# Kernel optimization log

Hardware: AMD Instinct MI355X
Metric: run time of the kernel (lower is better)

The kernel has to match this reference:

```python
import jax, jax.numpy as jnp
import numpy as np

B, NPG, C = 256, 256, 256  # graphs, nodes-per-graph, in_channels
MAX_LEN = 500


def _sinusoid_pe(max_len, c):
    pos = np.arange(max_len, dtype=np.float32)[:, None]
    div = np.exp(np.arange(0, c, 2, dtype=np.float32) * (-np.log(10000.0) / c))
    pe = np.zeros((max_len, c), np.float32)
    pe[:, 0::2] = np.sin(pos * div)
    pe[:, 1::2] = np.cos(pos * div)
    return jnp.asarray(pe)


def setup_inputs() -> dict:
    key = jax.random.key(0)
    ks = jax.random.split(key, 8)
    N = B * NPG
    x = jax.random.normal(ks[0], (N, C), jnp.float32)
    batch = jnp.repeat(jnp.arange(B, dtype=jnp.int32), NPG)
    # every other atom in each graph is an N/O atom -> 128 per graph
    on_index = (jnp.arange(B, dtype=jnp.int32)[:, None] * NPG
                + jnp.arange(0, NPG, 2, dtype=jnp.int32)[None, :]).reshape(-1)
    W1 = jax.random.normal(ks[1], (C, 256), jnp.float32) / np.sqrt(C)
    b1 = jnp.zeros((256,), jnp.float32)
    W2 = jax.random.normal(ks[2], (256, 128), jnp.float32) / np.sqrt(256.0)
    b2 = jnp.zeros((128,), jnp.float32)
    W3 = jax.random.normal(ks[3], (128, 64), jnp.float32) / np.sqrt(128.0)
    b3 = jnp.zeros((64,), jnp.float32)
    w_atom = jax.random.normal(ks[4], (64,), jnp.float32) / 8.0
    return {"x": x, "pe": _sinusoid_pe(MAX_LEN, C), "W1": W1, "b1": b1,
            "W2": W2, "b2": b2, "W3": W3, "b3": b3, "w_atom": w_atom,
            "batch": batch, "on_index": on_index, "ratio": 16}


def _lrelu(z):
    return jnp.where(z > 0, z, 0.1 * z)


def reference(x, pe, W1, b1, W2, b2, W3, b3, w_atom, batch, on_index, ratio):
    N = x.shape[0]
    bsz = int(batch[-1]) + 1
    num_nodes = jax.ops.segment_sum(jnp.ones_like(batch), batch, num_segments=bsz)
    cum = jnp.concatenate([jnp.zeros((1,), batch.dtype), jnp.cumsum(num_nodes)[:-1]])
    n = int(num_nodes.max())  # max_num_nodes
    idx_in_graph = jnp.arange(N, dtype=batch.dtype) - cum[batch]
    # positional encoding (dropout = identity in eval)
    xp = x + pe[idx_in_graph]
    # scoring MLP
    h = _lrelu(xp @ W1 + b1)
    h = _lrelu(h @ W2 + b2)
    h = _lrelu(h @ W3 + b3)
    score = jnp.tanh((h * w_atom).sum(-1) / jnp.linalg.norm(w_atom))
    # dense-pack scores into [bsz, n] padded with -inf, sort descending per row
    dense_idx = jnp.arange(N, dtype=batch.dtype) - cum[batch] + batch * n
    dense = jnp.full((bsz * n,), jnp.finfo(x.dtype).min, x.dtype).at[dense_idx].set(score)
    order = jnp.argsort(-dense.reshape(bsz, n), axis=-1)       # perm within row
    ranks = jnp.argsort(order, axis=-1)                         # inverse perm
    pos_in_perm = (jnp.arange(bsz)[:, None] * n + ranks).reshape(-1)
    # positions (in the flattened perm) of N/O atoms, sorted -> grouped per graph
    on_par = dense_idx[on_index]                                # padded/parallel ids
    indices = jnp.sort(pos_in_perm[on_par])
    m = on_index.shape[0] // bsz                                # N/O atoms per graph (uniform here)
    k = min(int(ratio), m)                                      # k = min(ratio, on_num)
    pre_mask = (jnp.arange(bsz)[:, None] * m + jnp.arange(k)[None, :]).reshape(-1)
    mask = indices[pre_mask]
    # map padded indices back to global node ids (subtract cumulative void counts)
    void = n - num_nodes
    cum_void = jnp.concatenate([jnp.zeros((1,), batch.dtype), jnp.cumsum(void)[:-1]])
    perm_flat = (order + (jnp.arange(bsz) * n - cum_void)[:, None]).reshape(-1)
    perm = perm_flat[mask]
    x_top = (xp[perm] * score[perm][:, None]).reshape(bsz, int(ratio), -1)
    return (x_top, perm, score[on_index], on_index)
```

## Files before the change

### kernel.cpp

```cpp
#include <hip/hip_runtime.h>
#include <hip/hip_bf16.h>


typedef __attribute__((ext_vector_type(8))) short short8v;
typedef __attribute__((ext_vector_type(4))) float float4v;

#define W1P_OFF 0
#define W2P_OFF 131072
#define W3P_OFF 196608
#define SCORES_OFF 212992

static __device__ __forceinline__ float lrelu(float z) { return z > 0.0f ? z : 0.1f * z; }

static __device__ __forceinline__ short f2bf(float f) {
    union { float f; unsigned u; } v; v.f = f;
    const unsigned r = v.u + 0x7FFFu + ((v.u >> 16) & 1u);
    return (short)(r >> 16);
}

static __device__ __forceinline__ int sw_off(int row, int chunk, int within) {
    return row * 256 + ((chunk ^ (row & 7)) << 3) + within;
}

__global__ __launch_bounds__(256) void pack_kernel(
    const float* __restrict__ W1, const float* __restrict__ W2,
    const float* __restrict__ W3, short* __restrict__ ws)
{
    const int u = blockIdx.x * 256 + threadIdx.x;
    if (u >= 13312) return;
    const float* W; int N, unitBase, uu;
    short* dst;
    if (u < 8192)       { W = W1; N = 256; uu = u;         dst = ws + (W1P_OFF/2); unitBase = 8; }
    else if (u < 12288) { W = W2; N = 128; uu = u - 8192;  dst = ws + (W2P_OFF/2); unitBase = 8; }
    else                { W = W3; N = 64;  uu = u - 12288; dst = ws + (W3P_OFF/2); unitBase = 4; }
    const int perNt = unitBase * 64;
    const int nt   = uu / perNt;
    const int rem  = uu % perNt;
    const int ks   = rem / 64;
    const int lane = rem % 64;
    const int q = lane >> 4;
    const int n = nt * 16 + (lane & 15);
    short8v frag;
    #pragma unroll
    for (int j = 0; j < 8; ++j) {
        const int k = ks * 32 + q * 8 + j;
        frag[j] = f2bf(W[(size_t)k * N + n]);
    }
    *(short8v*)(dst + (size_t)uu * 8) = frag;
}

__global__ __launch_bounds__(256, 5) void mlp_score_kernel(
    const float* __restrict__ x, const float* __restrict__ pe,
    const float* __restrict__ b1, const float* __restrict__ b2,
    const float* __restrict__ b3, const float* __restrict__ w_atom,
    const int* __restrict__ on_index, const short* __restrict__ ws_pack,
    float* __restrict__ ws_scores,
    float* __restrict__ out_score, float* __restrict__ out_onidx)
{
    __shared__ __align__(16) short XP[32 * 256];
    __shared__ __align__(16) short H1[32 * 256];
    const int t   = threadIdx.x;
    const int m0  = blockIdx.x * 32;
    const int wid = t >> 6;
    const int lane = t & 63;
    const int q = lane >> 4;
    const int c = lane & 15;

    const short* W1p = ws_pack + (W1P_OFF / 2);
    const short* W2p = ws_pack + (W2P_OFF / 2);
    const short* W3p = ws_pack + (W3P_OFF / 2);

    #pragma unroll
    for (int i = 0; i < 4; ++i) {
        const int u = t + i * 256;
        const int r = u >> 5;
        const int ck = u & 31;
        const int k = ck << 3;
        const int node = on_index[m0 + r];
        const float4 xa = *(const float4*)(x + (size_t)node * 256 + k);
        const float4 xb = *(const float4*)(x + (size_t)node * 256 + k + 4);
        const float4 pa = *(const float4*)(pe + (size_t)(node & 255) * 256 + k);
        const float4 pb = *(const float4*)(pe + (size_t)(node & 255) * 256 + k + 4);
        short8v s;
        s[0] = f2bf(xa.x + pa.x); s[1] = f2bf(xa.y + pa.y);
        s[2] = f2bf(xa.z + pa.z); s[3] = f2bf(xa.w + pa.w);
        s[4] = f2bf(xb.x + pb.x); s[5] = f2bf(xb.y + pb.y);
        s[6] = f2bf(xb.z + pb.z); s[7] = f2bf(xb.w + pb.w);
        *(short8v*)(&XP[sw_off(r, ck, 0)]) = s;
    }
    __syncthreads();

    #pragma unroll
    for (int g = 0; g < 2; ++g) {
        const int ntA = wid * 4 + g * 2;
        float4v acc[2][2];
        #pragma unroll
        for (int nt = 0; nt < 2; ++nt) {
            const float bb = b1[(ntA + nt) * 16 + c];
            acc[0][nt] = (float4v){bb, bb, bb, bb};
            acc[1][nt] = (float4v){bb, bb, bb, bb};
        }
        #pragma unroll
        for (int ks = 0; ks < 8; ++ks) {
            const short8v a0 = *(const short8v*)(&XP[sw_off(c,      ks * 4 + q, 0)]);
            const short8v a1 = *(const short8v*)(&XP[sw_off(16 + c, ks * 4 + q, 0)]);
            #pragma unroll
            for (int nt = 0; nt < 2; ++nt) {
                const short8v b = *(const short8v*)(W1p + ((size_t)((ntA + nt) * 8 + ks) * 64 + lane) * 8);
                acc[0][nt] = __builtin_amdgcn_mfma_f32_16x16x32_bf16(a0, b, acc[0][nt], 0, 0, 0);
                acc[1][nt] = __builtin_amdgcn_mfma_f32_16x16x32_bf16(a1, b, acc[1][nt], 0, 0, 0);
            }
        }
        #pragma unroll
        for (int mt = 0; mt < 2; ++mt)
            #pragma unroll
            for (int nt = 0; nt < 2; ++nt)
                #pragma unroll
                for (int r = 0; r < 4; ++r) {
                    const int row = mt * 16 + q * 4 + r;
                    const int col = (ntA + nt) * 16 + c;
                    H1[sw_off(row, col >> 3, col & 7)] = f2bf(lrelu(acc[mt][nt][r]));
                }
    }
    __syncthreads();

    {
        const int nt0 = wid * 2;
        float4v acc[2][2];
        #pragma unroll
        for (int nt = 0; nt < 2; ++nt) {
            const float bb = b2[(nt0 + nt) * 16 + c];
            acc[0][nt] = (float4v){bb, bb, bb, bb};
            acc[1][nt] = (float4v){bb, bb, bb, bb};
        }
        #pragma unroll
        for (int ks = 0; ks < 8; ++ks) {
            const short8v a0 = *(const short8v*)(&H1[sw_off(c,      ks * 4 + q, 0)]);
            const short8v a1 = *(const short8v*)(&H1[sw_off(16 + c, ks * 4 + q, 0)]);
            #pragma unroll
            for (int nt = 0; nt < 2; ++nt) {
                const short8v b = *(const short8v*)(W2p + ((size_t)((nt0 + nt) * 8 + ks) * 64 + lane) * 8);
                acc[0][nt] = __builtin_amdgcn_mfma_f32_16x16x32_bf16(a0, b, acc[0][nt], 0, 0, 0);
                acc[1][nt] = __builtin_amdgcn_mfma_f32_16x16x32_bf16(a1, b, acc[1][nt], 0, 0, 0);
            }
        }
        __syncthreads();
        #pragma unroll
        for (int mt = 0; mt < 2; ++mt)
            #pragma unroll
            for (int nt = 0; nt < 2; ++nt)
                #pragma unroll
                for (int r = 0; r < 4; ++r) {
                    const int row = mt * 16 + q * 4 + r;
                    const int col = (nt0 + nt) * 16 + c;
                    XP[sw_off(row, col >> 3, col & 7)] = f2bf(lrelu(acc[mt][nt][r]));
                }
    }
    __syncthreads();

    {
        const int nt = wid;
        float4v acc[2];
        const float bb = b3[nt * 16 + c];
        acc[0] = (float4v){bb, bb, bb, bb};
        acc[1] = (float4v){bb, bb, bb, bb};
        #pragma unroll
        for (int ks = 0; ks < 4; ++ks) {
            const short8v a0 = *(const short8v*)(&XP[sw_off(c,      ks * 4 + q, 0)]);
            const short8v a1 = *(const short8v*)(&XP[sw_off(16 + c, ks * 4 + q, 0)]);
            const short8v b = *(const short8v*)(W3p + ((size_t)(nt * 4 + ks) * 64 + lane) * 8);
            acc[0] = __builtin_amdgcn_mfma_f32_16x16x32_bf16(a0, b, acc[0], 0, 0, 0);
            acc[1] = __builtin_amdgcn_mfma_f32_16x16x32_bf16(a1, b, acc[1], 0, 0, 0);
        }
        float* H3F = (float*)H1;
        #pragma unroll
        for (int mt = 0; mt < 2; ++mt)
            #pragma unroll
            for (int r = 0; r < 4; ++r)
                H3F[(mt * 16 + q * 4 + r) * 68 + nt * 16 + c] = lrelu(acc[mt][r]);
    }
    __syncthreads();

    {
        const float* H3F = (const float*)H1;
        float* PART = (float*)XP;
        const int r = t >> 3, p = t & 7;
        float s = 0.0f;
        #pragma unroll
        for (int j = 0; j < 8; ++j) s += H3F[r * 68 + p * 8 + j] * w_atom[p * 8 + j];
        PART[t] = s;
        __syncthreads();
        if (t < 32) {
            float sum = 0.0f;
            #pragma unroll
            for (int pp = 0; pp < 8; ++pp) sum += PART[t * 8 + pp];
            float n2 = 0.0f;
            for (int cc = 0; cc < 64; ++cc) { const float w = w_atom[cc]; n2 += w * w; }
            const float sc = tanhf(sum / sqrtf(n2));
            const int m = m0 + t;
            ws_scores[m] = sc;
            out_score[m] = sc;
            out_onidx[m] = (float)on_index[m];
        }
    }
}

__global__ __launch_bounds__(256) void topk_gather_kernel(
    const float* __restrict__ x, const float* __restrict__ pe,
    const float* __restrict__ ws_scores, const int* __restrict__ on_index,
    float* __restrict__ out_perm, float* __restrict__ out_xtop)
{
    __shared__ float s[128];
    __shared__ int   sel_node[16];
    __shared__ float sel_sc[16];
    const int g = blockIdx.x, t = threadIdx.x;
    if (t < 128) s[t] = ws_scores[g * 128 + t];
    __syncthreads();
    if (t < 128) {
        const float sj = s[t];
        int rank = 0;
        for (int i = 0; i < 128; ++i) {
            const float si = s[i];
            rank += (si > sj) || (si == sj && i < t);
        }
        if (rank < 16) {
            const int node = on_index[g * 128 + t];
            sel_node[rank] = node;
            sel_sc[rank]   = sj;
            out_perm[g * 16 + rank] = (float)node;
        }
    }
    __syncthreads();
    #pragma unroll
    for (int k = 0; k < 16; ++k) {
        const int node = sel_node[k];
        const float sc = sel_sc[k];
        const float v = (x[(size_t)node * 256 + t] + pe[(size_t)(node & 255) * 256 + t]) * sc;
        out_xtop[((size_t)(g * 16 + k)) * 256 + t] = v;
    }
}

extern "C" void kernel_launch(void* const* d_in, const int* in_sizes, int n_in,
                              void* d_out, int out_size, void* d_ws, size_t ws_size,
                              hipStream_t stream)
{
    const float* x   = (const float*)d_in[0];
    const float* pe  = (const float*)d_in[1];
    const float* W1  = (const float*)d_in[2];
    const float* b1  = (const float*)d_in[3];
    const float* W2  = (const float*)d_in[4];
    const float* b2  = (const float*)d_in[5];
    const float* W3  = (const float*)d_in[6];
    const float* b3  = (const float*)d_in[7];
    const float* wa  = (const float*)d_in[8];
    const int* on_index = (const int*)d_in[10];

    float* out = (float*)d_out;
    float* out_xtop  = out;
    float* out_perm  = out + 1048576;
    float* out_score = out + 1048576 + 4096;
    float* out_onidx = out + 1048576 + 4096 + 32768;

    short* ws_pack   = (short*)d_ws;
    float* ws_scores = (float*)((char*)d_ws + SCORES_OFF);

    hipLaunchKernelGGL(pack_kernel, dim3(52), dim3(256), 0, stream, W1, W2, W3, ws_pack);
    hipLaunchKernelGGL(mlp_score_kernel, dim3(1024), dim3(256), 0, stream,
                       x, pe, b1, b2, b3, wa, on_index, (const short*)ws_pack,
                       ws_scores, out_score, out_onidx);
    hipLaunchKernelGGL(topk_gather_kernel, dim3(256), dim3(256), 0, stream,
                       x, pe, ws_scores, on_index, out_perm, out_xtop);
}
```

Measured before the change: 129.7 us.

## Double MLP row tile to 64 nodes per 512-thread block for weight reuse

```diff
diff --git a/kernel.cpp b/kernel.cpp
--- a/kernel.cpp
+++ b/kernel.cpp
@@ -49,7 +49,7 @@
     *(short8v*)(dst + (size_t)uu * 8) = frag;
 }
 
-__global__ __launch_bounds__(256, 5) void mlp_score_kernel(
+__global__ __launch_bounds__(512, 4) void mlp_score_kernel(
     const float* __restrict__ x, const float* __restrict__ pe,
     const float* __restrict__ b1, const float* __restrict__ b2,
     const float* __restrict__ b3, const float* __restrict__ w_atom,
@@ -57,10 +57,10 @@
     float* __restrict__ ws_scores,
     float* __restrict__ out_score, float* __restrict__ out_onidx)
 {
-    __shared__ __align__(16) short XP[32 * 256];
-    __shared__ __align__(16) short H1[32 * 256];
+    __shared__ __align__(16) short XP[64 * 256];
+    __shared__ __align__(16) short H1[64 * 256];
     const int t   = threadIdx.x;
-    const int m0  = blockIdx.x * 32;
+    const int m0  = blockIdx.x * 64;
     const int wid = t >> 6;
     const int lane = t & 63;
     const int q = lane >> 4;
@@ -72,7 +72,7 @@
 
     #pragma unroll
     for (int i = 0; i < 4; ++i) {
-        const int u = t + i * 256;
+        const int u = t + i * 512;
         const int r = u >> 5;
         const int ck = u & 31;
         const int k = ck << 3;
@@ -92,83 +92,69 @@
 
     #pragma unroll
     for (int g = 0; g < 2; ++g) {
-        const int ntA = wid * 4 + g * 2;
-        float4v acc[2][2];
-        #pragma unroll
-        for (int nt = 0; nt < 2; ++nt) {
-            const float bb = b1[(ntA + nt) * 16 + c];
-            acc[0][nt] = (float4v){bb, bb, bb, bb};
-            acc[1][nt] = (float4v){bb, bb, bb, bb};
-        }
+        const int nt = wid * 2 + g;
+        float4v acc[4];
+        const float bb = b1[nt * 16 + c];
+        #pragma unroll
+        for (int mt = 0; mt < 4; ++mt) acc[mt] = (float4v){bb, bb, bb, bb};
         #pragma unroll
         for (int ks = 0; ks < 8; ++ks) {
-            const short8v a0 = *(const short8v*)(&XP[sw_off(c,      ks * 4 + q, 0)]);
-            const short8v a1 = *(const short8v*)(&XP[sw_off(16 + c, ks * 4 + q, 0)]);
-            #pragma unroll
-            for (int nt = 0; nt < 2; ++nt) {
-                const short8v b = *(const short8v*)(W1p + ((size_t)((ntA + nt) * 8 + ks) * 64 + lane) * 8);
-                acc[0][nt] = __builtin_amdgcn_mfma_f32_16x16x32_bf16(a0, b, acc[0][nt], 0, 0, 0);
-                acc[1][nt] = __builtin_amdgcn_mfma_f32_16x16x32_bf16(a1, b, acc[1][nt], 0, 0, 0);
-            }
-        }
-        #pragma unroll
-        for (int mt = 0; mt < 2; ++mt)
-            #pragma unroll
-            for (int nt = 0; nt < 2; ++nt)
-                #pragma unroll
-                for (int r = 0; r < 4; ++r) {
-                    const int row = mt * 16 + q * 4 + r;
-                    const int col = (ntA + nt) * 16 + c;
-                    H1[sw_off(row, col >> 3, col & 7)] = f2bf(lrelu(acc[mt][nt][r]));
-                }
-    }
-    __syncthreads();
-
-    {
-        const int nt0 = wid * 2;
-        float4v acc[2][2];
-        #pragma unroll
-        for (int nt = 0; nt < 2; ++nt) {
-            const float bb = b2[(nt0 + nt) * 16 + c];
-            acc[0][nt] = (float4v){bb, bb, bb, bb};
-            acc[1][nt] = (float4v){bb, bb, bb, bb};
-        }
-        #pragma unroll
-        for (int ks = 0; ks < 8; ++ks) {
-            const short8v a0 = *(const short8v*)(&H1[sw_off(c,      ks * 4 + q, 0)]);
-            const short8v a1 = *(const short8v*)(&H1[sw_off(16 + c, ks * 4 + q, 0)]);
-            #pragma unroll
-            for (int nt = 0; nt < 2; ++nt) {
-                const short8v b = *(const short8v*)(W2p + ((size_t)((nt0 + nt) * 8 + ks) * 64 + lane) * 8);
-                acc[0][nt] = __builtin_amdgcn_mfma_f32_16x16x32_bf16(a0, b, acc[0][nt], 0, 0, 0);
-                acc[1][nt] = __builtin_amdgcn_mfma_f32_16x16x32_bf16(a1, b, acc[1][nt], 0, 0, 0);
-            }
-        }
-        __syncthreads();
-        #pragma unroll
-        for (int mt = 0; mt < 2; ++mt)
-            #pragma unroll
-            for (int nt = 0; nt < 2; ++nt)
-                #pragma unroll
-                for (int r = 0; r < 4; ++r) {
-                    const int row = mt * 16 + q * 4 + r;
-                    const int col = (nt0 + nt) * 16 + c;
-                    XP[sw_off(row, col >> 3, col & 7)] = f2bf(lrelu(acc[mt][nt][r]));
-                }
+            const short8v b = *(const short8v*)(W1p + ((size_t)(nt * 8 + ks) * 64 + lane) * 8);
+            #pragma unroll
+            for (int mt = 0; mt < 4; ++mt) {
+                const short8v a = *(const short8v*)(&XP[sw_off(mt * 16 + c, ks * 4 + q, 0)]);
+                acc[mt] = __builtin_amdgcn_mfma_f32_16x16x32_bf16(a, b, acc[mt], 0, 0, 0);
+            }
+        }
+        #pragma unroll
+        for (int mt = 0; mt < 4; ++mt)
+            #pragma unroll
+            for (int r = 0; r < 4; ++r) {
+                const int row = mt * 16 + q * 4 + r;
+                const int col = nt * 16 + c;
+                H1[sw_off(row, col >> 3, col & 7)] = f2bf(lrelu(acc[mt][r]));
+            }
     }
     __syncthreads();
 
     {
         const int nt = wid;
+        float4v acc[4];
+        const float bb = b2[nt * 16 + c];
+        #pragma unroll
+        for (int mt = 0; mt < 4; ++mt) acc[mt] = (float4v){bb, bb, bb, bb};
+        #pragma unroll
+        for (int ks = 0; ks < 8; ++ks) {
+            const short8v b = *(const short8v*)(W2p + ((size_t)(nt * 8 + ks) * 64 + lane) * 8);
+            #pragma unroll
+            for (int mt = 0; mt < 4; ++mt) {
+                const short8v a = *(const short8v*)(&H1[sw_off(mt * 16 + c, ks * 4 + q, 0)]);
+                acc[mt] = __builtin_amdgcn_mfma_f32_16x16x32_bf16(a, b, acc[mt], 0, 0, 0);
+            }
+        }
+        #pragma unroll
+        for (int mt = 0; mt < 4; ++mt)
+            #pragma unroll
+            for (int r = 0; r < 4; ++r) {
+                const int row = mt * 16 + q * 4 + r;
+                const int col = nt * 16 + c;
+                XP[sw_off(row, col >> 3, col & 7)] = f2bf(lrelu(acc[mt][r]));
+            }
+    }
+    __syncthreads();
+
+    {
+        const int nt  = wid & 3;
+        const int mt0 = (wid >> 2) * 2;
         float4v acc[2];
         const float bb = b3[nt * 16 + c];
         acc[0] = (float4v){bb, bb, bb, bb};
         acc[1] = (float4v){bb, bb, bb, bb};
         #pragma unroll
         for (int ks = 0; ks < 4; ++ks) {
-            const short8v a0 = *(const short8v*)(&XP[sw_off(c,      ks * 4 + q, 0)]);
-            const short8v a1 = *(const short8v*)(&XP[sw_off(16 + c, ks * 4 + q, 0)]);
             const short8v b = *(const short8v*)(W3p + ((size_t)(nt * 4 + ks) * 64 + lane) * 8);
+            const short8v a0 = *(const short8v*)(&XP[sw_off((mt0 + 0) * 16 + c, ks * 4 + q, 0)]);
+            const short8v a1 = *(const short8v*)(&XP[sw_off((mt0 + 1) * 16 + c, ks * 4 + q, 0)]);
             acc[0] = __builtin_amdgcn_mfma_f32_16x16x32_bf16(a0, b, acc[0], 0, 0, 0);
             acc[1] = __builtin_amdgcn_mfma_f32_16x16x32_bf16(a1, b, acc[1], 0, 0, 0);
         }
@@ -177,7 +163,7 @@
         for (int mt = 0; mt < 2; ++mt)
             #pragma unroll
             for (int r = 0; r < 4; ++r)
-                H3F[(mt * 16 + q * 4 + r) * 68 + nt * 16 + c] = lrelu(acc[mt][r]);
+                H3F[((mt0 + mt) * 16 + q * 4 + r) * 68 + nt * 16 + c] = lrelu(acc[mt][r]);
     }
     __syncthreads();
 
@@ -190,7 +176,7 @@
         for (int j = 0; j < 8; ++j) s += H3F[r * 68 + p * 8 + j] * w_atom[p * 8 + j];
         PART[t] = s;
         __syncthreads();
-        if (t < 32) {
+        if (t < 64) {
             float sum = 0.0f;
             #pragma unroll
             for (int pp = 0; pp < 8; ++pp) sum += PART[t * 8 + pp];
@@ -265,7 +251,7 @@
     float* ws_scores = (float*)((char*)d_ws + SCORES_OFF);
 
     hipLaunchKernelGGL(pack_kernel, dim3(52), dim3(256), 0, stream, W1, W2, W3, ws_pack);
-    hipLaunchKernelGGL(mlp_score_kernel, dim3(1024), dim3(256), 0, stream,
+    hipLaunchKernelGGL(mlp_score_kernel, dim3(512), dim3(512), 0, stream,
                        x, pe, b1, b2, b3, wa, on_index, (const short*)ws_pack,
                        ws_scores, out_score, out_onidx);
     hipLaunchKernelGGL(topk_gather_kernel, dim3(256), dim3(256), 0, stream,
```

New measurement: 126.1 us. 2.8% less time.
